# Performance work log

Hardware: AMD Instinct MI355X
Metric: run time of the kernel (lower is better)

## Reference

```python
import jax, jax.numpy as jnp
import numpy as np

# Static configuration (matches init_kwargs / input_specs)
NUM_SEQS = 8          # sequences in the batch
H = 32                # query heads
H_KV = 8              # kv heads (GQA group = 4)
D = 128               # head dim
MEM_BLK = 64          # paged-cache block size (tokens per cache block)
CTX = 2048            # cached context length per sequence (uniform)
Q = 64                # new (diffusion-block) tokens per sequence
MAX_BLKS = CTX // MEM_BLK   # 32 blocks per sequence in block_tables
N_BLOCKS = 512        # total cache blocks in the pool
SCALE = 1.0 / float(np.sqrt(D))


def setup_inputs() -> dict:
    key = jax.random.key(0)
    k0, k1, k2, k3, k4 = jax.random.split(key, 5)
    T = NUM_SEQS * Q  # total new tokens (flat ragged layout)
    q = jax.random.normal(k0, (T, H, D), dtype=jnp.float32)
    k = jax.random.normal(k1, (T, H_KV, D), dtype=jnp.float32)
    v = jax.random.normal(k2, (T, H_KV, D), dtype=jnp.float32)
    k_cache = jax.random.normal(k3, (N_BLOCKS, MEM_BLK, H_KV, D), dtype=jnp.float32)
    v_cache = jax.random.normal(k4, (N_BLOCKS, MEM_BLK, H_KV, D), dtype=jnp.float32)
    # sequence s owns cache blocks [s*MAX_BLKS, (s+1)*MAX_BLKS)
    block_tables = jnp.arange(NUM_SEQS * MAX_BLKS, dtype=jnp.int32).reshape(NUM_SEQS, MAX_BLKS)
    # new tokens are written into freshly allocated slots beyond the context blocks
    slot_mapping = NUM_SEQS * MAX_BLKS * MEM_BLK + jnp.arange(T, dtype=jnp.int32)
    return {"q": q, "k": k, "v": v, "k_cache": k_cache, "v_cache": v_cache,
            "block_tables": block_tables, "slot_mapping": slot_mapping}


def reference(q, k, v, k_cache, v_cache, block_tables, slot_mapping):
    # --- store_kvcache: scatter new k/v rows into flat cache slots ---
    kc_flat = k_cache.reshape(-1, H_KV, D).at[slot_mapping].set(k)
    vc_flat = v_cache.reshape(-1, H_KV, D).at[slot_mapping].set(v)
    kc = kc_flat.reshape(N_BLOCKS, MEM_BLK, H_KV, D)
    vc = vc_flat.reshape(N_BLOCKS, MEM_BLK, H_KV, D)

    # --- load_kvcache: block-table indexed gather of context, concat new kv ---
    # ctx_k/ctx_v: [S, CTX, H_KV, D]
    ctx_k = kc[block_tables].reshape(NUM_SEQS, MAX_BLKS * MEM_BLK, H_KV, D)[:, :CTX]
    ctx_v = vc[block_tables].reshape(NUM_SEQS, MAX_BLKS * MEM_BLK, H_KV, D)[:, :CTX]
    k_new = k.reshape(NUM_SEQS, Q, H_KV, D)
    v_new = v.reshape(NUM_SEQS, Q, H_KV, D)
    k_full = jnp.concatenate([ctx_k, k_new], axis=1)  # [S, CTX+Q, H_KV, D]
    v_full = jnp.concatenate([ctx_v, v_new], axis=1)

    # --- flex attention with GQA: diffusion block attends to full context +
    #     bidirectionally within its own new block ---
    G = H // H_KV
    qg = q.reshape(NUM_SEQS, Q, H_KV, G, D)
    # scores: [S, H_KV, G, Q, CTX+Q]
    scores = jnp.einsum("sqhgd,skhd->shgqk", qg, k_full) * SCALE
    attn = jax.nn.softmax(scores, axis=-1)
    out = jnp.einsum("shgqk,skhd->sqhgd", attn, v_full)  # [S, Q, H_KV, G, D]
    return out.reshape(NUM_SEQS * Q, H, D)
```

## Files before the change

### kernel.cpp

```cpp
#include <hip/hip_runtime.h>
#include <hip/hip_bf16.h>


typedef float  f32x16 __attribute__((ext_vector_type(16)));
typedef short  bf16x8 __attribute__((ext_vector_type(8)));

__device__ __forceinline__ unsigned pkbf(float lo, float hi) {
    union { __hip_bfloat162 h; unsigned u; } t;
    t.h.x = __float2bfloat16(lo);
    t.h.y = __float2bfloat16(hi);
    return t.u;
}
__device__ __forceinline__ float bf2f(unsigned short u) {
    return __uint_as_float((unsigned)u << 16);
}

#define BARRIER_LGKM() asm volatile("s_waitcnt lgkmcnt(0)\n\ts_barrier" ::: "memory")

#define OWS_ELEMS (4u * 64u * 256u * 128u)

__launch_bounds__(512, 1)
__global__ void attn_part(const float* __restrict__ qg,
                          const float* __restrict__ kin,
                          const float* __restrict__ vin,
                          const float* __restrict__ kcache,
                          const float* __restrict__ vcache,
                          const int*   __restrict__ bt,
                          __hip_bfloat16* __restrict__ Ows,
                          float* __restrict__ Lws)
{
    __shared__ __align__(16) unsigned char smem[32768];

    const int bid   = blockIdx.x;
    const int grp   = bid & 63;
    const int slice = bid >> 6;
    const int s     = grp >> 3;
    const int hkv   = grp & 7;

    const int tid  = threadIdx.x;
    const int w    = tid >> 6;
    const int lane = tid & 63;
    const int l32  = lane & 31;
    const int hi2  = lane >> 5;
    const int g    = w >> 1;
    const int qh   = w & 1;

    unsigned char* KB = smem;
    unsigned char* VB = smem + 16384;

    const float QSCALE = 0.08838834764831845f * 1.44269504088896340736f;

    bf16x8 aq[8];
    {
        const float* qp =
            qg + (size_t)((s * 64 + qh * 32 + l32) * 32 + hkv * 4 + g) * 128;
#pragma unroll
        for (int dc = 0; dc < 8; ++dc) {
            const float* p = qp + dc * 16 + hi2 * 8;
            const float4 f0 = *(const float4*)(p);
            const float4 f1 = *(const float4*)(p + 4);
            uint4 tt = make_uint4(pkbf(f0.x * QSCALE, f0.y * QSCALE),
                                  pkbf(f0.z * QSCALE, f0.w * QSCALE),
                                  pkbf(f1.x * QSCALE, f1.y * QSCALE),
                                  pkbf(f1.z * QSCALE, f1.w * QSCALE));
            aq[dc] = __builtin_bit_cast(bf16x8, tt);
        }
    }

    f32x16 acco[4];
#pragma unroll
    for (int dc = 0; dc < 4; ++dc) acco[dc] = (f32x16)0.f;
    float lsum = 0.f;

    const int vd  = tid & 127;
    const int vkg = tid >> 7;

    float4 kregA[2], kregB[2];
    float  vregA[8], vregB[8];

    const int tile0 = (slice < 2) ? slice * 17 : 34 + (slice - 2) * 16;
    const int nt    = (slice < 2) ? 17 : 16;

    auto src_for = [&](int T, const float*& ks, const float*& vs) {
        if (T < 64) {
            const int blk = bt[s * 32 + (T >> 1)];
            const size_t base = (size_t)blk * 65536 + (size_t)(T & 1) * 32768 + hkv * 128;
            ks = kcache + base; vs = vcache + base;
        } else {
            const size_t base = (size_t)(s * 64 + (T & 1) * 32) * 1024 + hkv * 128;
            ks = kin + base; vs = vin + base;
        }
    };

#define LOAD_REGS(SET, T)                                                         \
    do {                                                                          \
        const float *ks_, *vs_;                                                   \
        src_for((T), ks_, vs_);                                                   \
        _Pragma("unroll")                                                         \
        for (int i = 0; i < 2; ++i) {                                             \
            const int f = tid + 512 * i;                                          \
            kreg##SET[i] = *(const float4*)(ks_ + (size_t)(f >> 5) * 1024 + (f & 31) * 4); \
        }                                                                         \
        _Pragma("unroll")                                                         \
        for (int j = 0; j < 8; ++j)                                               \
            vreg##SET[j] = vs_[(size_t)(vkg * 8 + j) * 1024 + vd];                \
    } while (0)

#define WRITE_LDS(SET, BUF)                                                       \
    do {                                                                          \
        unsigned char* K_ = KB + (BUF) * 8192;                                    \
        unsigned char* V_ = VB + (BUF) * 8192;                                    \
        _Pragma("unroll")                                                         \
        for (int i = 0; i < 2; ++i) {                                             \
            const int f  = tid + 512 * i;                                         \
            const int kv = f >> 5;                                                \
            const int dk = f & 31;                                                \
            const int Xs = dk ^ ((kv & 15) << 1);                                 \
            *(uint2*)(K_ + kv * 256 + Xs * 8) =                                   \
                make_uint2(pkbf(kreg##SET[i].x, kreg##SET[i].y),                  \
                           pkbf(kreg##SET[i].z, kreg##SET[i].w));                 \
        }                                                                         \
        const int u_ = vkg ^ ((vd >> 1) & 3);                                     \
        *(uint4*)(V_ + vd * 64 + u_ * 16) =                                       \
            make_uint4(pkbf(vreg##SET[0], vreg##SET[1]),                          \
                       pkbf(vreg##SET[2], vreg##SET[3]),                          \
                       pkbf(vreg##SET[4], vreg##SET[5]),                          \
                       pkbf(vreg##SET[6], vreg##SET[7]));                         \
    } while (0)

    const int vq = (l32 >> 1) & 3;

    auto compute = [&](int buf) {
        const unsigned char* K = KB + buf * 8192;
        const unsigned char* V = VB + buf * 8192;

        f32x16 sc = (f32x16)0.f;
#pragma unroll
        for (int dc = 0; dc < 8; ++dc) {
            const int u = (dc * 2 + hi2) ^ (l32 & 15);
            const bf16x8 ak = *(const bf16x8*)(K + l32 * 256 + u * 16);
            sc = __builtin_amdgcn_mfma_f32_32x32x16_bf16(ak, aq[dc], sc, 0, 0, 0);
        }

        float p[16];
#pragma unroll
        for (int r = 0; r < 16; ++r) {
            p[r] = __builtin_amdgcn_exp2f(sc[r]);
            lsum += p[r];
        }

        unsigned A0 = pkbf(p[0],  p[1]),  A1 = pkbf(p[2],  p[3]);
        unsigned B0 = pkbf(p[4],  p[5]),  B1 = pkbf(p[6],  p[7]);
        unsigned C0 = pkbf(p[8],  p[9]),  C1 = pkbf(p[10], p[11]);
        unsigned D0 = pkbf(p[12], p[13]), D1 = pkbf(p[14], p[15]);
        asm volatile("v_permlane32_swap_b32 %0, %1" : "+v"(A0), "+v"(B0));
        asm volatile("v_permlane32_swap_b32 %0, %1" : "+v"(A1), "+v"(B1));
        asm volatile("v_permlane32_swap_b32 %0, %1" : "+v"(C0), "+v"(D0));
        asm volatile("v_permlane32_swap_b32 %0, %1" : "+v"(C1), "+v"(D1));
        bf16x8 pa[2];
        {
            uint4 t0 = make_uint4(A0, A1, B0, B1);
            uint4 t1 = make_uint4(C0, C1, D0, D1);
            pa[0] = __builtin_bit_cast(bf16x8, t0);
            pa[1] = __builtin_bit_cast(bf16x8, t1);
        }

#pragma unroll
        for (int kk = 0; kk < 2; ++kk)
#pragma unroll
            for (int d2 = 0; d2 < 4; ++d2) {
                const int u = (kk * 2 + hi2) ^ vq;
                const bf16x8 bv = *(const bf16x8*)(V + (d2 * 32 + l32) * 64 + u * 16);
                acco[d2] = __builtin_amdgcn_mfma_f32_32x32x16_bf16(pa[kk], bv, acco[d2], 0, 0, 0);
            }
    };

    LOAD_REGS(A, tile0);
    WRITE_LDS(A, 0);
    LOAD_REGS(B, tile0 + 1);
    LOAD_REGS(A, tile0 + 2);

    int tt = 0;
    while (true) {
        BARRIER_LGKM();
        if (tt + 1 < nt) WRITE_LDS(B, 1);
        if (tt + 3 < nt) LOAD_REGS(B, tile0 + tt + 3);
        compute(0);
        if (tt + 1 >= nt) break;

        BARRIER_LGKM();
        if (tt + 2 < nt) WRITE_LDS(A, 0);
        if (tt + 4 < nt) LOAD_REGS(A, tile0 + tt + 4);
        compute(1);
        tt += 2;
        if (tt >= nt) break;
    }

    const float lt = lsum + __shfl_xor(lsum, 32);
    const size_t gq = (size_t)(slice * 64 + grp) * 256 + w * 32;
    if (hi2 == 0) Lws[gq + l32] = lt;
    __hip_bfloat16* Od = Ows + gq * 128;
#pragma unroll
    for (int dc = 0; dc < 4; ++dc)
#pragma unroll
        for (int r = 0; r < 16; ++r) {
            const int qiw = (r & 3) + 8 * (r >> 2) + 4 * hi2;
            Od[(size_t)qiw * 128 + dc * 32 + l32] = __float2bfloat16(acco[dc][r]);
        }
}

__launch_bounds__(256)
__global__ void attn_combine(const __hip_bfloat16* __restrict__ Ows,
                             const float* __restrict__ Lws,
                             float* __restrict__ out)
{
    const int idx = blockIdx.x * 256 + threadIdx.x;
    const int dq  = idx & 31;
    const int qr  = (idx >> 5) & 255;
    const int grp = idx >> 13;
    const int s = grp >> 3, hkv = grp & 7;
    const int g = qr >> 6, qtok = qr & 63;

    float4 acc = make_float4(0.f, 0.f, 0.f, 0.f);
    float  l   = 0.f;
#pragma unroll
    for (int sl = 0; sl < 4; ++sl) {
        const size_t base = (size_t)(sl * 64 + grp) * 256 + qr;
        const ushort4 p = *(const ushort4*)(Ows + base * 128 + dq * 4);
        acc.x += bf2f(p.x); acc.y += bf2f(p.y);
        acc.z += bf2f(p.z); acc.w += bf2f(p.w);
        l += Lws[base];
    }
    const float inv = 1.0f / l;
    float4 o = make_float4(acc.x * inv, acc.y * inv, acc.z * inv, acc.w * inv);
    *(float4*)(out + ((size_t)((s * 64 + qtok) * 32 + hkv * 4 + g)) * 128 + dq * 4) = o;
}

extern "C" void kernel_launch(void* const* d_in, const int* in_sizes, int n_in,
                              void* d_out, int out_size, void* d_ws, size_t ws_size,
                              hipStream_t stream)
{
    const float* q  = (const float*)d_in[0];
    const float* k  = (const float*)d_in[1];
    const float* v  = (const float*)d_in[2];
    const float* kc = (const float*)d_in[3];
    const float* vc = (const float*)d_in[4];
    const int*   bt = (const int*)d_in[5];
    __hip_bfloat16* Ows = (__hip_bfloat16*)d_ws;
    float* Lws = (float*)((char*)d_ws + (size_t)OWS_ELEMS * 2);
    float* o   = (float*)d_out;

    attn_part<<<dim3(256), dim3(512), 0, stream>>>(q, k, v, kc, vc, bt, Ows, Lws);
    attn_combine<<<dim3(2048), dim3(256), 0, stream>>>(Ows, Lws, o);
}
```

Measured before the change: 41.64 us.

## Fuse split-KV combine into partial kernel via last-block atomic counter

Removes the separate combine kernel launch. Each of the four slice blocks for a group bumps an atomic counter after writing its partial output and denominator, and the last block to arrive reduces all slices and writes the final output. This saves a kernel launch and its dependency gap, but adds a memset launch, threadfences, and a serialized tail in which only 64 blocks do the reduction.

```diff
diff --git a/kernel.cpp b/kernel.cpp
--- a/kernel.cpp
+++ b/kernel.cpp
@@ -18,6 +18,8 @@
 #define BARRIER_LGKM() asm volatile("s_waitcnt lgkmcnt(0)\n\ts_barrier" ::: "memory")
 
 #define OWS_ELEMS (4u * 64u * 256u * 128u)
+#define LWS_BYTES (4u * 64u * 256u * 4u)
+#define CNT_OFF   ((size_t)OWS_ELEMS * 2 + LWS_BYTES)
 
 __launch_bounds__(512, 1)
 __global__ void attn_part(const float* __restrict__ qg,
@@ -27,9 +29,12 @@
                           const float* __restrict__ vcache,
                           const int*   __restrict__ bt,
                           __hip_bfloat16* __restrict__ Ows,
-                          float* __restrict__ Lws)
+                          float* __restrict__ Lws,
+                          unsigned* __restrict__ cnt,
+                          float* __restrict__ out)
 {
     __shared__ __align__(16) unsigned char smem[32768];
+    __shared__ int amLast;
 
     const int bid   = blockIdx.x;
     const int grp   = bid & 63;
@@ -207,33 +212,38 @@
             const int qiw = (r & 3) + 8 * (r >> 2) + 4 * hi2;
             Od[(size_t)qiw * 128 + dc * 32 + l32] = __float2bfloat16(acco[dc][r]);
         }
-}
-
-__launch_bounds__(256)
-__global__ void attn_combine(const __hip_bfloat16* __restrict__ Ows,
-                             const float* __restrict__ Lws,
-                             float* __restrict__ out)
-{
-    const int idx = blockIdx.x * 256 + threadIdx.x;
-    const int dq  = idx & 31;
-    const int qr  = (idx >> 5) & 255;
-    const int grp = idx >> 13;
-    const int s = grp >> 3, hkv = grp & 7;
-    const int g = qr >> 6, qtok = qr & 63;
-
-    float4 acc = make_float4(0.f, 0.f, 0.f, 0.f);
-    float  l   = 0.f;
-#pragma unroll
-    for (int sl = 0; sl < 4; ++sl) {
-        const size_t base = (size_t)(sl * 64 + grp) * 256 + qr;
-        const ushort4 p = *(const ushort4*)(Ows + base * 128 + dq * 4);
-        acc.x += bf2f(p.x); acc.y += bf2f(p.y);
-        acc.z += bf2f(p.z); acc.w += bf2f(p.w);
-        l += Lws[base];
-    }
-    const float inv = 1.0f / l;
-    float4 o = make_float4(acc.x * inv, acc.y * inv, acc.z * inv, acc.w * inv);
-    *(float4*)(out + ((size_t)((s * 64 + qtok) * 32 + hkv * 4 + g)) * 128 + dq * 4) = o;
+
+    __threadfence();
+    __syncthreads();
+    if (tid == 0) {
+        const unsigned old = __hip_atomic_fetch_add(&cnt[grp], 1u,
+                                 __ATOMIC_ACQ_REL, __HIP_MEMORY_SCOPE_AGENT);
+        amLast = (old == 3u);
+    }
+    __syncthreads();
+    if (!amLast) return;
+    __threadfence();
+
+#pragma unroll
+    for (int it = 0; it < 16; ++it) {
+        const int li = it * 512 + tid;
+        const int dq = li & 31;
+        const int qr = li >> 5;
+        float4 acc = make_float4(0.f, 0.f, 0.f, 0.f);
+        float  l   = 0.f;
+#pragma unroll
+        for (int sl = 0; sl < 4; ++sl) {
+            const size_t base = (size_t)(sl * 64 + grp) * 256 + qr;
+            const ushort4 p = *(const ushort4*)(Ows + base * 128 + dq * 4);
+            acc.x += bf2f(p.x); acc.y += bf2f(p.y);
+            acc.z += bf2f(p.z); acc.w += bf2f(p.w);
+            l += Lws[base];
+        }
+        const float inv = 1.0f / l;
+        const int gg = qr >> 6, qtok = qr & 63;
+        float4 o = make_float4(acc.x * inv, acc.y * inv, acc.z * inv, acc.w * inv);
+        *(float4*)(out + ((size_t)((s * 64 + qtok) * 32 + hkv * 4 + gg)) * 128 + dq * 4) = o;
+    }
 }
 
 extern "C" void kernel_launch(void* const* d_in, const int* in_sizes, int n_in,
@@ -247,9 +257,11 @@
     const float* vc = (const float*)d_in[4];
     const int*   bt = (const int*)d_in[5];
     __hip_bfloat16* Ows = (__hip_bfloat16*)d_ws;
-    float* Lws = (float*)((char*)d_ws + (size_t)OWS_ELEMS * 2);
-    float* o   = (float*)d_out;
-
-    attn_part<<<dim3(256), dim3(512), 0, stream>>>(q, k, v, kc, vc, bt, Ows, Lws);
-    attn_combine<<<dim3(2048), dim3(256), 0, stream>>>(Ows, Lws, o);
-}
+    float*    Lws = (float*)((char*)d_ws + (size_t)OWS_ELEMS * 2);
+    unsigned* cnt = (unsigned*)((char*)d_ws + CNT_OFF);
+    float*    o   = (float*)d_out;
+
+    hipMemsetAsync(cnt, 0, 64 * sizeof(unsigned), stream);
+    attn_part<<<dim3(256), dim3(512), 0, stream>>>(q, k, v, kc, vc, bt,
+                                                   Ows, Lws, cnt, o);
+}
```

New measurement: 126.2 us. 203% more time.
